# Optimization experiments

Hardware: AMD Instinct MI355X
Metric: run time of the kernel (lower is better)

Reference implementation:

```python
import jax, jax.numpy as jnp
import numpy as np

H, DH, M, ITERS = 8, 64, 256, 6   # heads, dim_head, num_landmarks, pinv iters
DIM = H * DH                      # 512
KERNEL = 33                       # residual depthwise conv kernel


def setup_inputs() -> dict:
    key = jax.random.key(0)
    ks = jax.random.split(key, 5)
    b, n = 2, 8192                # n multiple of M -> no divisibility padding
    x = jax.random.normal(ks[0], (b, n, DIM), jnp.float32)
    ln_gamma = jnp.ones((DIM,), jnp.float32)
    ln_beta = jnp.zeros((DIM,), jnp.float32)
    w_qkv = jax.random.normal(ks[1], (DIM, 3 * DIM), jnp.float32) * 0.02
    w_out = jax.random.normal(ks[2], (DIM, DIM), jnp.float32) * 0.02
    b_out = jnp.zeros((DIM,), jnp.float32)
    res_kernel = jax.random.normal(ks[3], (H, 1, KERNEL, 1), jnp.float32) * 0.02
    return {"x": x, "ln_gamma": ln_gamma, "ln_beta": ln_beta, "w_qkv": w_qkv,
            "w_out": w_out, "b_out": b_out, "res_kernel": res_kernel}


def _pinv(a, iters):
    # lucidrains moore_penrose_iter_pinv (Newton-Schulz iteration)
    abs_a = jnp.abs(a)
    scale = abs_a.sum(-1).max() * abs_a.sum(-2).max()
    z = jnp.swapaxes(a, -1, -2) / scale
    I = jnp.eye(a.shape[-1], dtype=a.dtype)
    for _ in range(iters):
        az = a @ z
        z = 0.25 * z @ (13.0 * I - az @ (15.0 * I - az @ (7.0 * I - az)))
    return z


def reference(x, ln_gamma, ln_beta, w_qkv, w_out, b_out, res_kernel):
    b, n, d = x.shape
    # pre-LayerNorm (eps 1e-5)
    mu = jnp.mean(x, -1, keepdims=True)
    var = jnp.var(x, -1, keepdims=True)
    xn = (x - mu) * jax.lax.rsqrt(var + 1e-5) * ln_gamma + ln_beta
    # qkv projection (bias-free)
    q, k, v = jnp.split(xn @ w_qkv, 3, axis=-1)
    to_heads = lambda t: t.reshape(b, n, H, DH).transpose(0, 2, 1, 3)  # b h n d
    q, k, v = to_heads(q), to_heads(k), to_heads(v)
    q = q * (DH ** -0.5)
    # landmarks: mean over groups of l consecutive tokens ('(m l) d -> m d')
    l = n // M
    q_l = q.reshape(b, H, M, l, DH).mean(3)  # b h M d
    k_l = k.reshape(b, H, M, l, DH).mean(3)
    sim1 = jnp.einsum('bhnd,bhmd->bhnm', q, k_l)      # queries vs k-landmarks
    sim2 = jnp.einsum('bhid,bhjd->bhij', q_l, k_l)    # landmarks vs landmarks
    sim3 = jnp.einsum('bhmd,bhnd->bhmn', q_l, k)      # q-landmarks vs keys
    a1 = jax.nn.softmax(sim1, axis=-1)
    a2 = jax.nn.softmax(sim2, axis=-1)
    a3 = jax.nn.softmax(sim3, axis=-1)
    a2_inv = _pinv(a2, ITERS)
    out = (a1 @ a2_inv) @ (a3 @ v)  # b h n d
    # residual depthwise conv over the sequence axis (Conv2d kernel (33,1), groups=H)
    pad = KERNEL // 2
    out = out + jax.lax.conv_general_dilated(
        v, res_kernel, (1, 1), [(pad, pad), (0, 0)],
        dimension_numbers=('NCHW', 'OIHW', 'NCHW'), feature_group_count=H)
    out = out.transpose(0, 2, 1, 3).reshape(b, n, d)
    out = out @ w_out + b_out  # to_out Linear (dropout inactive at eval)
    return x + out             # TransLayer residual
```

## Files before the change

kernel.cpp:

```cpp
#include <hip/hip_runtime.h>
#include <math.h>

#define H_ 8
#define DH_ 64
#define DIM_ 512
#define M_ 256
#define N_ 8192
#define BH_ 16
#define LG_ 32
#define KC_ 33
#define CH_ 16
#define NTI_ 8

typedef __attribute__((ext_vector_type(8))) short bf16x8;
typedef __attribute__((ext_vector_type(4))) short s16x4;
typedef __attribute__((ext_vector_type(4))) float f32x4;

__device__ __forceinline__ short f2bf(float f) {
  unsigned u = __float_as_uint(f);
  unsigned r = (u + 0x7FFF + ((u >> 16) & 1)) >> 16;
  return (short)r;
}
__device__ __forceinline__ float bf2f(short s) {
  return __uint_as_float(((unsigned)(unsigned short)s) << 16);
}

__device__ __forceinline__ void mfma_nt_core(const short* __restrict__ A,
                                             const short* __restrict__ Bt, int K,
                                             int m0, int n0, size_t lda, size_t ldb,
                                             f32x4 acc[4][4], short* As, short* Bs) {
  const int tid = threadIdx.x;
  const int wave = tid >> 6, lane = tid & 63;
  const int wr = (wave >> 1) * 64, wc = (wave & 1) * 64;
  const int mi = lane & 15, quad = lane >> 4;
  for (int k0 = 0; k0 < K; k0 += 32) {
#pragma unroll
    for (int t = 0; t < 2; ++t) {
      const int cbase = (t * 4 + wave) * 64;
      const int chunk = cbase + lane;
      const int row = chunk >> 2, cc = (chunk & 3) * 8;
      __builtin_amdgcn_global_load_lds(
          (const __attribute__((address_space(1))) void*)(A + (size_t)(m0 + row) * lda + k0 + cc),
          (__attribute__((address_space(3))) void*)(As + (size_t)cbase * 8), 16, 0, 0);
      __builtin_amdgcn_global_load_lds(
          (const __attribute__((address_space(1))) void*)(Bt + (size_t)(n0 + row) * ldb + k0 + cc),
          (__attribute__((address_space(3))) void*)(Bs + (size_t)cbase * 8), 16, 0, 0);
    }
    __syncthreads();
    bf16x8 af[4], bf[4];
#pragma unroll
    for (int i = 0; i < 4; ++i)
      af[i] = *(const bf16x8*)&As[(wr + i * 16 + mi) * 32 + quad * 8];
#pragma unroll
    for (int j = 0; j < 4; ++j)
      bf[j] = *(const bf16x8*)&Bs[(wc + j * 16 + mi) * 32 + quad * 8];
#pragma unroll
    for (int i = 0; i < 4; ++i)
#pragma unroll
      for (int j = 0; j < 4; ++j)
        acc[i][j] = __builtin_amdgcn_mfma_f32_16x16x32_bf16(af[i], bf[j], acc[i][j], 0, 0, 0);
    __syncthreads();
  }
}

__global__ __launch_bounds__(256) void qkv_mfma(const short* __restrict__ xnb,
                                                const short* __restrict__ wt,
                                                short* __restrict__ qb, short* __restrict__ kb,
                                                short* __restrict__ vb) {
  __shared__ short As[128 * 32], Bs[128 * 32];
  f32x4 acc[4][4] = {};
  const int m0 = blockIdx.x * 128, n0 = blockIdx.y * 128;
  mfma_nt_core(xnb, wt, DIM_, m0, n0, DIM_, DIM_, acc, As, Bs);
  const int wave = threadIdx.x >> 6, lane = threadIdx.x & 63;
  const int wr = (wave >> 1) * 64, wc = (wave & 1) * 64;
  const int mi = lane & 15, quad = lane >> 4;
  const int which = n0 >> 9;
  short* dst = which == 0 ? qb : which == 1 ? kb : vb;
  const float sc = which == 0 ? 0.125f : 1.0f;
#pragma unroll
  for (int j = 0; j < 4; ++j) {
    const int col = n0 + wc + j * 16 + mi;
    const int h = (col >> 6) & 7, d = col & 63;
#pragma unroll
    for (int i = 0; i < 4; ++i) {
#pragma unroll
      for (int r = 0; r < 4; ++r) {
        const int row = m0 + wr + i * 16 + quad * 4 + r;
        const int b = row >> 13, t = row & (N_ - 1);
        dst[((size_t)(b * H_ + h) * N_ + t) * DH_ + d] = f2bf(acc[i][j][r] * sc);
      }
    }
  }
}

__global__ __launch_bounds__(256) void final_mfma(const short* __restrict__ omb,
                                                  const short* __restrict__ wt,
                                                  const float* __restrict__ x,
                                                  const float* __restrict__ bout,
                                                  float* __restrict__ y) {
  __shared__ short As[128 * 32], Bs[128 * 32];
  f32x4 acc[4][4] = {};
  const int m0 = blockIdx.x * 128, n0 = blockIdx.y * 128;
  mfma_nt_core(omb, wt, DIM_, m0, n0, DIM_, DIM_, acc, As, Bs);
  const int wave = threadIdx.x >> 6, lane = threadIdx.x & 63;
  const int wr = (wave >> 1) * 64, wc = (wave & 1) * 64;
  const int mi = lane & 15, quad = lane >> 4;
#pragma unroll
  for (int j = 0; j < 4; ++j) {
    const int col = n0 + wc + j * 16 + mi;
    const float bo = bout[col];
#pragma unroll
    for (int i = 0; i < 4; ++i) {
#pragma unroll
      for (int r = 0; r < 4; ++r) {
        const int row = m0 + wr + i * 16 + quad * 4 + r;
        y[(size_t)row * DIM_ + col] = acc[i][j][r] + x[(size_t)row * DIM_ + col] + bo;
      }
    }
  }
}

__global__ __launch_bounds__(256) void convt_kernel(const float* __restrict__ in,
                                                    short* __restrict__ out, int K, int N) {
  __shared__ float tile[32][33];
  const int n0 = blockIdx.x * 32, k0 = blockIdx.y * 32;
  const int tx = threadIdx.x & 31, ty = threadIdx.x >> 5;
  for (int r = ty; r < 32; r += 8) tile[r][tx] = in[(size_t)(k0 + r) * N + n0 + tx];
  __syncthreads();
  for (int r = ty; r < 32; r += 8) out[(size_t)(n0 + r) * K + k0 + tx] = f2bf(tile[tx][r]);
}

__global__ __launch_bounds__(256) void vt_kernel(const short* __restrict__ vb,
                                                 short* __restrict__ vtb) {
  __shared__ short tile[32][33];
  const int t0 = blockIdx.x * 32, d0 = blockIdx.y * 32, bh = blockIdx.z;
  const int tx = threadIdx.x & 31, ty = threadIdx.x >> 5;
  for (int r = ty; r < 32; r += 8)
    tile[r][tx] = vb[((size_t)bh * N_ + t0 + r) * DH_ + d0 + tx];
  __syncthreads();
  for (int r = ty; r < 32; r += 8)
    vtb[((size_t)bh * DH_ + d0 + r) * N_ + t0 + tx] = tile[tx][r];
}

__global__ __launch_bounds__(128) void ln_kernel(const float* __restrict__ x,
                                                 const float* __restrict__ gamma,
                                                 const float* __restrict__ beta,
                                                 short* __restrict__ xnb) {
  const int row = blockIdx.x, tid = threadIdx.x;
  const float4 v = ((const float4*)(x + (size_t)row * DIM_))[tid];
  float s = v.x + v.y + v.z + v.w;
  float ss = v.x * v.x + v.y * v.y + v.z * v.z + v.w * v.w;
  __shared__ float r1[128], r2[128];
  r1[tid] = s;
  r2[tid] = ss;
  __syncthreads();
  for (int off = 64; off > 0; off >>= 1) {
    if (tid < off) {
      r1[tid] += r1[tid + off];
      r2[tid] += r2[tid + off];
    }
    __syncthreads();
  }
  const float mu = r1[0] * (1.0f / DIM_);
  const float var = r2[0] * (1.0f / DIM_) - mu * mu;
  const float rs = rsqrtf(var + 1e-5f);
  const float4 g = ((const float4*)gamma)[tid];
  const float4 bb = ((const float4*)beta)[tid];
  s16x4 o = {f2bf((v.x - mu) * rs * g.x + bb.x), f2bf((v.y - mu) * rs * g.y + bb.y),
             f2bf((v.z - mu) * rs * g.z + bb.z), f2bf((v.w - mu) * rs * g.w + bb.w)};
  ((s16x4*)(xnb + (size_t)row * DIM_))[tid] = o;
}

__global__ __launch_bounds__(256) void landmark_kernel(const short* __restrict__ qb,
                                                       const short* __restrict__ kb,
                                                       float* __restrict__ ql,
                                                       float* __restrict__ kl,
                                                       short* __restrict__ qlb,
                                                       short* __restrict__ klb) {
  const int idx = blockIdx.x * 256 + threadIdx.x;
  const int d = idx & (DH_ - 1);
  const int m = (idx >> 6) & (M_ - 1);
  const int bh = idx >> 14;
  const size_t base = ((size_t)bh * N_ + m * LG_) * DH_ + d;
  float sq = 0.f, sk = 0.f;
#pragma unroll 8
  for (int t = 0; t < LG_; ++t) {
    sq += bf2f(qb[base + (size_t)t * DH_]);
    sk += bf2f(kb[base + (size_t)t * DH_]);
  }
  sq *= (1.0f / LG_);
  sk *= (1.0f / LG_);
  ql[idx] = sq;
  kl[idx] = sk;
  qlb[idx] = f2bf(sq);
  klb[idx] = f2bf(sk);
}

__global__ __launch_bounds__(256) void sim2_softmax(const float* __restrict__ ql,
                                                    const float* __restrict__ kl,
                                                    float* __restrict__ a2,
                                                    short* __restrict__ a2b) {
  const int i = blockIdx.x, bh = blockIdx.y, j = threadIdx.x;
  __shared__ float qrow[DH_];
  if (j < DH_) qrow[j] = ql[((size_t)bh * M_ + i) * DH_ + j];
  __syncthreads();
  const float* kr = kl + ((size_t)bh * M_ + j) * DH_;
  float s = 0.f;
#pragma unroll 16
  for (int d = 0; d < DH_; ++d) s += qrow[d] * kr[d];
  __shared__ float red[256];
  red[j] = s;
  __syncthreads();
  for (int off = 128; off > 0; off >>= 1) {
    if (j < off) red[j] = fmaxf(red[j], red[j + off]);
    __syncthreads();
  }
  const float mx = red[0];
  __syncthreads();
  const float e = expf(s - mx);
  red[j] = e;
  __syncthreads();
  for (int off = 128; off > 0; off >>= 1) {
    if (j < off) red[j] += red[j + off];
    __syncthreads();
  }
  const float out = e / red[0];
  a2[((size_t)bh * M_ + i) * M_ + j] = out;
  a2b[((size_t)bh * M_ + i) * M_ + j] = f2bf(out);
}

__global__ __launch_bounds__(256) void colmax_kernel(const float* __restrict__ a2,
                                                     unsigned int* __restrict__ scalebits) {
  const int bh = blockIdx.x, j = threadIdx.x;
  const float* mat = a2 + (size_t)bh * M_ * M_;
  float s = 0.f;
  for (int i = 0; i < M_; ++i) s += fabsf(mat[i * M_ + j]);
  __shared__ float red[256];
  red[j] = s;
  __syncthreads();
  for (int off = 128; off > 0; off >>= 1) {
    if (j < off) red[j] = fmaxf(red[j], red[j + off]);
    __syncthreads();
  }
  if (j == 0) atomicMax(scalebits, __float_as_uint(red[0]));
}

__global__ __launch_bounds__(256) void transpose_scale(const float* __restrict__ a2,
                                                       short* __restrict__ z0b,
                                                       const unsigned int* __restrict__ scalebits) {
  const float inv = 1.0f / __uint_as_float(*scalebits);
  const int idx = blockIdx.x * 256 + threadIdx.x;
  const int j = idx & (M_ - 1), i = (idx >> 8) & (M_ - 1), bh = idx >> 16;
  z0b[idx] = f2bf(a2[((size_t)bh * M_ + j) * M_ + i] * inv);
}

__device__ __forceinline__ void ns_core(const short* __restrict__ A, const short* __restrict__ B,
                                        int m0, int n0, short* Bs, f32x4 acc[4]) {
  const int tid = threadIdx.x, wave = tid >> 6, lane = tid & 63;
  const int mi = lane & 15, quad = lane >> 4;
  const int bkk = tid & 31, g = tid >> 5;
  bf16x8 bv[8];
#pragma unroll
  for (int kc = 0; kc < 8; ++kc)
    bv[kc] = *(const bf16x8*)(B + (size_t)(kc * 32 + bkk) * M_ + n0 + g * 8);
  const short* arow = A + (size_t)(m0 + wave * 16 + mi) * M_;
  bf16x8 af[8];
#pragma unroll
  for (int k0 = 0; k0 < 8; ++k0)
    af[k0] = *(const bf16x8*)(arow + k0 * 32 + quad * 8);
#pragma unroll
  for (int kc = 0; kc < 8; ++kc)
#pragma unroll
    for (int e = 0; e < 8; ++e)
      Bs[(g * 8 + e) * 260 + kc * 32 + bkk] = bv[kc][e];
  __syncthreads();
#pragma unroll
  for (int k0 = 0; k0 < 8; ++k0) {
#pragma unroll
    for (int j = 0; j < 4; ++j) {
      union { bf16x8 v; s16x4 h[2]; } bfr;
      const short* bp = &Bs[(j * 16 + mi) * 260 + k0 * 32 + quad * 8];
      bfr.h[0] = *(const s16x4*)bp;
      bfr.h[1] = *(const s16x4*)(bp + 4);
      acc[j] = __builtin_amdgcn_mfma_f32_16x16x32_bf16(af[k0], bfr.v, acc[j], 0, 0, 0);
    }
  }
}

__device__ __forceinline__ int ns_remap() {
  const int lin = blockIdx.y * 16 + blockIdx.x;
  return (lin & 7) * (gridDim.y << 1) + (lin >> 3);
}

__global__ __launch_bounds__(256) void ns_gemm0(const short* __restrict__ A,
                                                const short* __restrict__ B,
                                                short* __restrict__ C) {
  __shared__ short Bs[64 * 260];
  const int id = ns_remap();
  const int bx = id & 15, by = id >> 4;
  const int m0 = (bx >> 2) * 64, n0 = (bx & 3) * 64;
  const size_t mo = (size_t)by * (M_ * M_);
  f32x4 acc[4] = {};
  ns_core(A + mo, B + mo, m0, n0, Bs, acc);
  const int wave = threadIdx.x >> 6, lane = threadIdx.x & 63;
  const int mi = lane & 15, quad = lane >> 4;
#pragma unroll
  for (int j = 0; j < 4; ++j)
#pragma unroll
    for (int r = 0; r < 4; ++r) {
      const int row = m0 + wave * 16 + quad * 4 + r, col = n0 + j * 16 + mi;
      C[mo + (size_t)row * M_ + col] = f2bf(acc[j][r]);
    }
}

__global__ __launch_bounds__(256) void ns_stageA(const short* __restrict__ z,
                                                 const short* __restrict__ y,
                                                 short* __restrict__ p1,
                                                 short* __restrict__ y2,
                                                 short* __restrict__ w) {
  __shared__ short Bs[64 * 260];
  const int id = ns_remap();
  const int bx = id & 15, by = id >> 4;
  const int m0 = (bx >> 2) * 64, n0 = (bx & 3) * 64;
  const int sel = by & 1;
  const size_t mo = (size_t)(by >> 1) * (M_ * M_);
  f32x4 acc[4] = {};
  ns_core((sel ? y : z) + mo, y + mo, m0, n0, Bs, acc);
  const int wave = threadIdx.x >> 6, lane = threadIdx.x & 63;
  const int mi = lane & 15, quad = lane >> 4;
#pragma unroll
  for (int j = 0; j < 4; ++j)
#pragma unroll
    for (int r = 0; r < 4; ++r) {
      const int row = m0 + wave * 16 + quad * 4 + r, col = n0 + j * 16 + mi;
      const size_t idx = mo + (size_t)row * M_ + col;
      if (sel) {
        y2[idx] = f2bf(acc[j][r]);
        w[idx] = f2bf(1.75f * bf2f(y[idx]) - 0.25f * acc[j][r]);
      } else {
        p1[idx] = f2bf(acc[j][r]);
      }
    }
}

__global__ __launch_bounds__(256) void ns_stageB(const short* __restrict__ p1,
                                                 const short* __restrict__ y2,
                                                 const short* __restrict__ w,
                                                 const short* __restrict__ z,
                                                 const short* __restrict__ y,
                                                 short* __restrict__ zo,
                                                 short* __restrict__ yo,
                                                 float* __restrict__ zf, int zonly) {
  __shared__ short Bs[64 * 260];
  const int id = ns_remap();
  const int bx = id & 15, by = id >> 4;
  const int m0 = (bx >> 2) * 64, n0 = (bx & 3) * 64;
  const int sel = zonly ? 0 : (by & 1);
  const size_t mo = (size_t)(zonly ? by : (by >> 1)) * (M_ * M_);
  f32x4 acc[4] = {};
  ns_core((sel ? y2 : p1) + mo, w + mo, m0, n0, Bs, acc);
  const int wave = threadIdx.x >> 6, lane = threadIdx.x & 63;
  const int mi = lane & 15, quad = lane >> 4;
#pragma unroll
  for (int j = 0; j < 4; ++j)
#pragma unroll
    for (int r = 0; r < 4; ++r) {
      const int row = m0 + wave * 16 + quad * 4 + r, col = n0 + j * 16 + mi;
      const size_t idx = mo + (size_t)row * M_ + col;
      if (sel) {
        yo[idx] = f2bf(3.25f * bf2f(y[idx]) - 3.75f * bf2f(y2[idx]) + acc[j][r]);
      } else {
        const float v = 3.25f * bf2f(z[idx]) - 3.75f * bf2f(p1[idx]) + acc[j][r];
        zo[idx] = f2bf(v);
        if (zf) zf[idx] = v;
      }
    }
}

__device__ __forceinline__ void mm_step(float (*As)[68], float (*Bs)[68],
                                        int tr, int tc, float acc[4][4]) {
#pragma unroll
  for (int kk = 0; kk < 16; ++kk) {
    const float4 a4 = *(const float4*)&As[kk][tr * 4];
    const float4 b4 = *(const float4*)&Bs[kk][tc * 4];
    const float a[4] = {a4.x, a4.y, a4.z, a4.w};
    const float b[4] = {b4.x, b4.y, b4.z, b4.w};
#pragma unroll
    for (int i = 0; i < 4; ++i)
#pragma unroll
      for (int j = 0; j < 4; ++j) acc[i][j] = fmaf(a[i], b[j], acc[i][j]);
  }
}

__device__ __forceinline__ void load_a_tile(const float* A, int lda, int m0, int k0,
                                            int tid, float (*As)[68]) {
  const int r = tid >> 2, kq = tid & 3;
  const float4 a4 = *(const float4*)(A + (size_t)(m0 + r) * lda + k0 + kq * 4);
  As[kq * 4 + 0][r] = a4.x;
  As[kq * 4 + 1][r] = a4.y;
  As[kq * 4 + 2][r] = a4.z;
  As[kq * 4 + 3][r] = a4.w;
}

__device__ __forceinline__ void load_b_nn(const float* B, int ldb, int k0, int n0,
                                          int tid, float (*Bs)[68]) {
  const int kr = tid >> 4, c4 = tid & 15;
  const float4 b4 = *(const float4*)(B + (size_t)(k0 + kr) * ldb + n0 + c4 * 4);
  *(float4*)&Bs[kr][c4 * 4] = b4;
}

__global__ __launch_bounds__(256) void gemm_nn64(const float* __restrict__ A, int lda,
                                                 long long strideA,
                                                 const float* __restrict__ B, long long strideB,
                                                 float* __restrict__ C, long long strideC,
                                                 int kchunk) {
  const int bz = blockIdx.z;
  A += (size_t)bz * strideA;
  B += (size_t)bz * strideB;
  C += (size_t)bz * strideC;
  const int m0 = blockIdx.x * 64;
  const int tid = threadIdx.x, tr = tid >> 4, tc = tid & 15;
  __shared__ float As[16][68], Bs[16][68];
  float acc[4][4] = {};
  for (int k0 = 0; k0 < kchunk; k0 += 16) {
    load_a_tile(A, lda, m0, k0, tid, As);
    load_b_nn(B, DH_, k0, 0, tid, Bs);
    __syncthreads();
    mm_step(As, Bs, tr, tc, acc);
    __syncthreads();
  }
#pragma unroll
  for (int i = 0; i < 4; ++i) {
    const int row = m0 + tr * 4 + i;
    *(float4*)(C + (size_t)row * DH_ + tc * 4) =
        make_float4(acc[i][0], acc[i][1], acc[i][2], acc[i][3]);
  }
}

__device__ __forceinline__ void stage_ks(const short* __restrict__ kb, int bh, int n0,
                                         int wave, int lane, short* ks) {
#pragma unroll
  for (int i = 0; i < 2; ++i) {
    const int cb = i * 256 + wave * 64;
    const int c = cb + lane;
    const int row = c >> 3, cc = c & 7;
    __builtin_amdgcn_global_load_lds(
        (const __attribute__((address_space(1))) void*)(
            kb + ((size_t)bh * N_ + n0 + row) * DH_ + ((cc ^ (row & 7)) * 8)),
        (__attribute__((address_space(3))) void*)(ks + (size_t)cb * 8), 16, 0, 0);
  }
}

__global__ __launch_bounds__(256) void a3_flash(const short* __restrict__ qlb,
                                                const short* __restrict__ kb,
                                                const short* __restrict__ vtb,
                                                float* __restrict__ Opart,
                                                float* __restrict__ mpart,
                                                float* __restrict__ lpart) {
  const int chunk = blockIdx.x, rt = blockIdx.y, bh = blockIdx.z;
  __shared__ short ks[64 * 64];
  __shared__ short ps[64 * 64];
  const int tid = threadIdx.x, wave = tid >> 6, lane = tid & 63;
  const int mi = lane & 15, quad = lane >> 4;
  const short* qrow = qlb + ((size_t)bh * M_ + rt * 64 + wave * 16 + mi) * DH_;
  const bf16x8 aq0 = *(const bf16x8*)(qrow + quad * 8);
  const bf16x8 aq1 = *(const bf16x8*)(qrow + 32 + quad * 8);
  float m[4] = {-INFINITY, -INFINITY, -INFINITY, -INFINITY};
  float l[4] = {0.f, 0.f, 0.f, 0.f};
  f32x4 o[4] = {};
  stage_ks(kb, bh, chunk * (N_ / CH_), wave, lane, ks);
  __syncthreads();
  for (int t = 0; t < NTI_; ++t) {
    const int n0 = chunk * (N_ / CH_) + t * 64;
    f32x4 s[4];
#pragma unroll
    for (int j = 0; j < 4; ++j) {
      const int row = j * 16 + mi;
      const bf16x8 b0 = *(const bf16x8*)&ks[row * 64 + ((quad ^ (row & 7)) * 8)];
      const bf16x8 b1 = *(const bf16x8*)&ks[row * 64 + (((quad + 4) ^ (row & 7)) * 8)];
      f32x4 z = {0.f, 0.f, 0.f, 0.f};
      z = __builtin_amdgcn_mfma_f32_16x16x32_bf16(aq0, b0, z, 0, 0, 0);
      s[j] = __builtin_amdgcn_mfma_f32_16x16x32_bf16(aq1, b1, z, 0, 0, 0);
    }
    __syncthreads();
    if (t + 1 < NTI_) stage_ks(kb, bh, n0 + 64, wave, lane, ks);
    float alpha[4];
#pragma unroll
    for (int r = 0; r < 4; ++r) {
      float v = fmaxf(fmaxf(s[0][r], s[1][r]), fmaxf(s[2][r], s[3][r]));
      v = fmaxf(v, __shfl_xor(v, 1, 64));
      v = fmaxf(v, __shfl_xor(v, 2, 64));
      v = fmaxf(v, __shfl_xor(v, 4, 64));
      v = fmaxf(v, __shfl_xor(v, 8, 64));
      const float mnew = fmaxf(m[r], v);
      alpha[r] = __expf(m[r] - mnew);
      m[r] = mnew;
    }
    float rs[4] = {0.f, 0.f, 0.f, 0.f};
#pragma unroll
    for (int j = 0; j < 4; ++j)
#pragma unroll
      for (int r = 0; r < 4; ++r) {
        const float p = __expf(s[j][r] - m[r]);
        rs[r] += p;
        const int prow = wave * 16 + quad * 4 + r;
        const int pcol = j * 16 + mi;
        ps[prow * 64 + (((pcol >> 3) ^ (prow & 7)) * 8) + (pcol & 7)] = f2bf(p);
      }
#pragma unroll
    for (int r = 0; r < 4; ++r) {
      float v = rs[r];
      v += __shfl_xor(v, 1, 64);
      v += __shfl_xor(v, 2, 64);
      v += __shfl_xor(v, 4, 64);
      v += __shfl_xor(v, 8, 64);
      l[r] = l[r] * alpha[r] + v;
#pragma unroll
      for (int j = 0; j < 4; ++j) o[j][r] *= alpha[r];
    }
    const int prow = wave * 16 + mi;
    const bf16x8 ap0 = *(const bf16x8*)&ps[prow * 64 + ((quad ^ (mi & 7)) * 8)];
    const bf16x8 ap1 = *(const bf16x8*)&ps[prow * 64 + (((quad + 4) ^ (mi & 7)) * 8)];
#pragma unroll
    for (int j = 0; j < 4; ++j) {
      const short* vp = vtb + ((size_t)bh * DH_ + j * 16 + mi) * N_ + n0;
      const bf16x8 b0 = *(const bf16x8*)(vp + quad * 8);
      const bf16x8 b1 = *(const bf16x8*)(vp + 32 + quad * 8);
      o[j] = __builtin_amdgcn_mfma_f32_16x16x32_bf16(ap0, b0, o[j], 0, 0, 0);
      o[j] = __builtin_amdgcn_mfma_f32_16x16x32_bf16(ap1, b1, o[j], 0, 0, 0);
    }
    __syncthreads();
  }
  const int p2 = bh * 4 + rt;
  float* Ob = Opart + ((size_t)chunk * 64 + p2) * 4096;
#pragma unroll
  for (int j = 0; j < 4; ++j)
#pragma unroll
    for (int r = 0; r < 4; ++r)
      Ob[(wave * 16 + quad * 4 + r) * 64 + j * 16 + mi] = o[j][r];
  if (mi == 0) {
#pragma unroll
    for (int r = 0; r < 4; ++r) {
      mpart[((size_t)chunk * 64 + p2) * 64 + wave * 16 + quad * 4 + r] = m[r];
      lpart[((size_t)chunk * 64 + p2) * 64 + wave * 16 + quad * 4 + r] = l[r];
    }
  }
}

__global__ __launch_bounds__(256) void a3_combine(const float* __restrict__ Opart,
                                                  const float* __restrict__ mpart,
                                                  const float* __restrict__ lpart,
                                                  float* __restrict__ a3v) {
  const int p2 = blockIdx.x, ds = blockIdx.y;
  const int bh = p2 >> 2, rt = p2 & 3;
  __shared__ float wgt[CH_][64];
  const int tid = threadIdx.x;
  if (tid < 64) {
    float mg = -INFINITY;
#pragma unroll
    for (int c = 0; c < CH_; ++c) mg = fmaxf(mg, mpart[((size_t)c * 64 + p2) * 64 + tid]);
    float e[CH_], lg = 0.f;
#pragma unroll
    for (int c = 0; c < CH_; ++c) {
      e[c] = __expf(mpart[((size_t)c * 64 + p2) * 64 + tid] - mg);
      lg += lpart[((size_t)c * 64 + p2) * 64 + tid] * e[c];
    }
    const float inv = 1.f / lg;
#pragma unroll
    for (int c = 0; c < CH_; ++c) wgt[c][tid] = e[c] * inv;
  }
  __syncthreads();
  for (int i = ds * 1024 + tid; i < ds * 1024 + 1024; i += 256) {
    const int row = i >> 6, d = i & 63;
    float s = 0.f;
#pragma unroll
    for (int c = 0; c < CH_; ++c) s += Opart[((size_t)c * 64 + p2) * 4096 + i] * wgt[c][row];
    a3v[((size_t)bh * M_ + rt * 64 + row) * DH_ + d] = s;
  }
}

__global__ __launch_bounds__(256) void w2t_kernel(const float* __restrict__ w2,
                                                  short* __restrict__ w2tb) {
  const int bh = blockIdx.x, tid = threadIdx.x;
  for (int i = tid; i < M_ * DH_; i += 256) {
    const int r = i >> 6, d = i & 63;
    w2tb[((size_t)bh * DH_ + d) * M_ + r] = f2bf(w2[(size_t)bh * M_ * DH_ + i]);
  }
}

__global__ __launch_bounds__(256, 5) void a1_conv(const short* __restrict__ qb,
                                                  const short* __restrict__ klb,
                                                  const short* __restrict__ w2tb,
                                                  const short* __restrict__ vtb,
                                                  const float* __restrict__ rk,
                                                  short* __restrict__ omb) {
  __shared__ __align__(16) char smem[20096];
  short* kls = (short*)smem;
  short* ps = (short*)smem;
  short* vwin = (short*)smem;
  short* band = (short*)(smem + 17920);
  const int bh = blockIdx.y, t0 = blockIdx.x * 64;
  const int b = bh >> 3, h = bh & 7;
  const int tid = threadIdx.x, wave = tid >> 6, lane = tid & 63;
  const int mi = lane & 15, quad = lane >> 4;

  const short* qrow = qb + ((size_t)bh * N_ + t0 + wave * 16 + mi) * DH_;
  const bf16x8 aq0 = *(const bf16x8*)(qrow + quad * 8);
  const bf16x8 aq1 = *(const bf16x8*)(qrow + 32 + quad * 8);

#pragma unroll
  for (int i = 0; i < 4; ++i) {
    const int idx = tid + i * 256;
    const int r = idx >> 6, c = idx & 63, u = c - r;
    band[r * 68 + c] = (u >= 0 && u < KC_) ? f2bf(rk[h * KC_ + u]) : (short)0;
  }

  f32x4 s[16] = {};
#pragma unroll
  for (int half = 0; half < 2; ++half) {
    if (half) __syncthreads();
#pragma unroll
    for (int i = 0; i < 4; ++i) {
      const int cb = i * 256 + wave * 64;
      const int c = cb + lane;
      const int row = c >> 3, cc = c & 7;
      __builtin_amdgcn_global_load_lds(
          (const __attribute__((address_space(1))) void*)(
              klb + ((size_t)bh * M_ + half * 128 + row) * DH_ + (cc ^ (row & 7)) * 8),
          (__attribute__((address_space(3))) void*)(kls + (size_t)cb * 8), 16, 0, 0);
    }
    __syncthreads();
#pragma unroll
    for (int f = 0; f < 8; ++f) {
      const int row = f * 16 + mi;
      const bf16x8 blo = *(const bf16x8*)&kls[row * 64 + ((quad ^ (row & 7)) * 8)];
      const bf16x8 bhi = *(const bf16x8*)&kls[row * 64 + (((quad + 4) ^ (row & 7)) * 8)];
      f32x4 z = __builtin_amdgcn_mfma_f32_16x16x32_bf16(aq0, blo, s[half * 8 + f], 0, 0, 0);
      s[half * 8 + f] = __builtin_amdgcn_mfma_f32_16x16x32_bf16(aq1, bhi, z, 0, 0, 0);
    }
  }
  float inv[4];
#pragma unroll
  for (int r = 0; r < 4; ++r) {
    float v = s[0][r];
#pragma unroll
    for (int f = 1; f < 16; ++f) v = fmaxf(v, s[f][r]);
    v = fmaxf(v, __shfl_xor(v, 1, 64));
    v = fmaxf(v, __shfl_xor(v, 2, 64));
    v = fmaxf(v, __shfl_xor(v, 4, 64));
    v = fmaxf(v, __shfl_xor(v, 8, 64));
    float sum = 0.f;
#pragma unroll
    for (int f = 0; f < 16; ++f) {
      const float p = __expf(s[f][r] - v);
      s[f][r] = p;
      sum += p;
    }
    sum += __shfl_xor(sum, 1, 64);
    sum += __shfl_xor(sum, 2, 64);
    sum += __shfl_xor(sum, 4, 64);
    sum += __shfl_xor(sum, 8, 64);
    inv[r] = 1.f / sum;
  }
  __syncthreads();

  f32x4 o[4] = {};
#pragma unroll
  for (int half = 0; half < 2; ++half) {
#pragma unroll
    for (int f = 0; f < 8; ++f)
#pragma unroll
      for (int r = 0; r < 4; ++r)
        ps[(wave * 16 + quad * 4 + r) * 140 + f * 16 + mi] = f2bf(s[half * 8 + f][r] * inv[r]);
#pragma unroll
    for (int k0 = 0; k0 < 4; ++k0) {
      union { bf16x8 v; s16x4 hh[2]; } ap;
      const short* pp = &ps[(wave * 16 + mi) * 140 + k0 * 32 + quad * 8];
      ap.hh[0] = *(const s16x4*)pp;
      ap.hh[1] = *(const s16x4*)(pp + 4);
#pragma unroll
      for (int j = 0; j < 4; ++j) {
        const bf16x8 bw = *(const bf16x8*)(w2tb + ((size_t)bh * DH_ + j * 16 + mi) * M_ +
                                           (half * 4 + k0) * 32 + quad * 8);
        o[j] = __builtin_amdgcn_mfma_f32_16x16x32_bf16(ap.v, bw, o[j], 0, 0, 0);
      }
    }
  }
  __syncthreads();

  {
    const int d = tid & 63, cg0 = tid >> 6;
    const short* vrow = vtb + ((size_t)bh * DH_ + d) * N_;
    for (int ch = cg0; ch < 14; ch += 4) {
      const int tbase = t0 - 16 + ch * 8;
      bf16x8 vv;
      if (tbase >= 0 && tbase + 8 <= N_) {
        vv = *(const bf16x8*)(vrow + tbase);
      } else {
#pragma unroll
        for (int e = 0; e < 8; ++e) {
          const int tt = tbase + e;
          vv[e] = (tt >= 0 && tt < N_) ? vrow[tt] : (short)0;
        }
      }
      *(bf16x8*)&vwin[d * 116 + ch * 8] = vv;
    }
  }
  __syncthreads();

#pragma unroll
  for (int ks = 0; ks < 2; ++ks) {
    union { bf16x8 v; s16x4 hh[2]; } ab;
    const short* bp = &band[mi * 68 + ks * 32 + quad * 8];
    ab.hh[0] = *(const s16x4*)bp;
    ab.hh[1] = *(const s16x4*)(bp + 4);
#pragma unroll
    for (int j = 0; j < 4; ++j) {
      union { bf16x8 v; s16x4 hh[2]; } bv;
      const short* vp = &vwin[(j * 16 + mi) * 116 + wave * 16 + ks * 32 + quad * 8];
      bv.hh[0] = *(const s16x4*)vp;
      bv.hh[1] = *(const s16x4*)(vp + 4);
      o[j] = __builtin_amdgcn_mfma_f32_16x16x32_bf16(ab.v, bv.v, o[j], 0, 0, 0);
    }
  }
#pragma unroll
  for (int j = 0; j < 4; ++j) {
    const int d = j * 16 + mi;
#pragma unroll
    for (int r = 0; r < 4; ++r) {
      const int t = t0 + wave * 16 + quad * 4 + r;
      omb[((size_t)(b * N_ + t)) * DIM_ + h * DH_ + d] = f2bf(o[j][r]);
    }
  }
}

extern "C" void kernel_launch(void* const* d_in, const int* in_sizes, int n_in,
                              void* d_out, int out_size, void* d_ws, size_t ws_size,
                              hipStream_t stream) {
  (void)in_sizes; (void)n_in; (void)out_size;
  const float* x = (const float*)d_in[0];
  const float* gamma = (const float*)d_in[1];
  const float* beta = (const float*)d_in[2];
  const float* wqkv = (const float*)d_in[3];
  const float* wout = (const float*)d_in[4];
  const float* bout = (const float*)d_in[5];
  const float* rk = (const float*)d_in[6];
  float* y = (float*)d_out;
  float* ws = (float*)d_ws;

  size_t o = 0;
  short* xnb = (short*)(ws + o);   o += (size_t)2 * N_ * DIM_ / 2;
  short* wqkvt = (short*)(ws + o); o += (size_t)3 * DIM_ * DIM_ / 2;
  short* woutt = (short*)(ws + o); o += (size_t)DIM_ * DIM_ / 2;
  short* qb = (short*)(ws + o);    o += (size_t)BH_ * N_ * DH_ / 2;
  short* kb = (short*)(ws + o);    o += (size_t)BH_ * N_ * DH_ / 2;
  short* vb = (short*)(ws + o);    o += (size_t)BH_ * N_ * DH_ / 2;
  short* vtb = (short*)(ws + o);   o += (size_t)BH_ * N_ * DH_ / 2;
  float* ql = ws + o;  o += (size_t)BH_ * M_ * DH_;
  float* kl = ws + o;  o += (size_t)BH_ * M_ * DH_;
  short* qlb = (short*)(ws + o); o += (size_t)BH_ * M_ * DH_ / 2;
  short* klb = (short*)(ws + o); o += (size_t)BH_ * M_ * DH_ / 2;
  float* a2 = ws + o;  o += (size_t)BH_ * M_ * M_;
  float* z0f = ws + o; o += (size_t)BH_ * M_ * M_;
  short* a2b = (short*)(ws + o); o += (size_t)BH_ * M_ * M_ / 2;
  short* zb0 = (short*)(ws + o); o += (size_t)BH_ * M_ * M_ / 2;
  short* zb1 = (short*)(ws + o); o += (size_t)BH_ * M_ * M_ / 2;
  short* yb0 = (short*)(ws + o); o += (size_t)BH_ * M_ * M_ / 2;
  short* yb1 = (short*)(ws + o); o += (size_t)BH_ * M_ * M_ / 2;
  short* p1b = (short*)(ws + o); o += (size_t)BH_ * M_ * M_ / 2;
  short* y2b = (short*)(ws + o); o += (size_t)BH_ * M_ * M_ / 2;
  short* wb  = (short*)(ws + o); o += (size_t)BH_ * M_ * M_ / 2;
  float* Opart = ws + o; o += (size_t)CH_ * 64 * 4096;
  float* mpart = ws + o; o += (size_t)CH_ * 64 * 64;
  float* lpart = ws + o; o += (size_t)CH_ * 64 * 64;
  float* a3v = ws + o; o += (size_t)BH_ * M_ * DH_;
  float* w2 = ws + o;  o += (size_t)BH_ * M_ * DH_;
  short* w2tb = (short*)(ws + o); o += (size_t)BH_ * M_ * DH_ / 2;
  short* omb = (short*)(ws + o);  o += (size_t)2 * N_ * DIM_ / 2;
  unsigned int* scalebits = (unsigned int*)(ws + o); o += 16;
  if (ws_size < o * sizeof(float)) return;

  (void)hipMemsetAsync(scalebits, 0, 64, stream);
  ln_kernel<<<2 * N_, 128, 0, stream>>>(x, gamma, beta, xnb);
  convt_kernel<<<dim3(3 * DIM_ / 32, DIM_ / 32), 256, 0, stream>>>(wqkv, wqkvt, DIM_, 3 * DIM_);
  convt_kernel<<<dim3(DIM_ / 32, DIM_ / 32), 256, 0, stream>>>(wout, woutt, DIM_, DIM_);
  qkv_mfma<<<dim3(2 * N_ / 128, 3 * DIM_ / 128), 256, 0, stream>>>(xnb, wqkvt, qb, kb, vb);
  vt_kernel<<<dim3(N_ / 32, 2, BH_), 256, 0, stream>>>(vb, vtb);

  landmark_kernel<<<BH_ * M_ * DH_ / 256, 256, 0, stream>>>(qb, kb, ql, kl, qlb, klb);
  sim2_softmax<<<dim3(M_, BH_), 256, 0, stream>>>(ql, kl, a2, a2b);
  colmax_kernel<<<BH_, 256, 0, stream>>>(a2, scalebits);
  transpose_scale<<<BH_ * M_ * M_ / 256, 256, 0, stream>>>(a2, zb0, scalebits);

  a3_flash<<<dim3(CH_, 4, BH_), 256, 0, stream>>>(qlb, kb, vtb, Opart, mpart, lpart);
  a3_combine<<<dim3(64, 4), 256, 0, stream>>>(Opart, mpart, lpart, a3v);

  ns_gemm0<<<dim3(16, BH_), 256, 0, stream>>>(a2b, zb0, yb0);
  short* zc = zb0; short* zn = zb1; short* yc = yb0; short* yn = yb1;
  for (int it = 0; it < 6; ++it) {
    const int last = (it == 5);
    ns_stageA<<<dim3(16, 2 * BH_), 256, 0, stream>>>(zc, yc, p1b, y2b, wb);
    ns_stageB<<<dim3(16, last ? BH_ : 2 * BH_), 256, 0, stream>>>(
        p1b, y2b, wb, zc, yc, zn, yn, last ? z0f : nullptr, last);
    short* t;
    t = zc; zc = zn; zn = t;
    t = yc; yc = yn; yn = t;
  }

  gemm_nn64<<<dim3(M_ / 64, 1, BH_), 256, 0, stream>>>(
      z0f, M_, (long long)M_ * M_, a3v, (long long)M_ * DH_, w2, (long long)M_ * DH_, M_);
  w2t_kernel<<<BH_, 256, 0, stream>>>(w2, w2tb);

  a1_conv<<<dim3(N_ / 64, BH_), 256, 0, stream>>>(qb, klb, w2tb, vtb, rk, omb);

  final_mfma<<<dim3(2 * N_ / 128, DIM_ / 128), 256, 0, stream>>>(omb, woutt, x, bout, y);
}
```

Measured before the change: 463.9 us.

## Double-buffer K/V tiles in a3_flash and restructure a1_conv loads and normalization

a3_flash now stages both K and V tiles into double-buffered LDS with async global-to-LDS loads. The next tile is prefetched while the current one is computed, and one barrier per iteration is dropped. The per-iteration row-sum shuffle reduction is deferred to a single reduction after the loop. a1_conv now loads all landmark keys in one pass, prefetches the V window into registers at kernel start, and applies the softmax normalization to the output accumulators instead of to P. This needs more LDS and a lower launch-bounds occupancy hint (5 to 4 blocks) in exchange for fewer barriers and better latency hiding.

Result: faster. 445.1 us (-4.1%).

```diff
diff --git a/kernel.cpp b/kernel.cpp
--- a/kernel.cpp
+++ b/kernel.cpp
@@ -451,6 +451,20 @@
   }
 }
 
+__device__ __forceinline__ void stage_vs(const short* __restrict__ vtb, int bh, int n0,
+                                         int wave, int lane, short* vs) {
+#pragma unroll
+  for (int i = 0; i < 2; ++i) {
+    const int cb = i * 256 + wave * 64;
+    const int c = cb + lane;
+    const int row = c >> 3, cc = c & 7;
+    __builtin_amdgcn_global_load_lds(
+        (const __attribute__((address_space(1))) void*)(
+            vtb + ((size_t)bh * DH_ + row) * N_ + n0 + ((cc ^ (row & 7)) * 8)),
+        (__attribute__((address_space(3))) void*)(vs + (size_t)cb * 8), 16, 0, 0);
+  }
+}
+
 __global__ __launch_bounds__(256) void a3_flash(const short* __restrict__ qlb,
                                                 const short* __restrict__ kb,
                                                 const short* __restrict__ vtb,
@@ -458,7 +472,8 @@
                                                 float* __restrict__ mpart,
                                                 float* __restrict__ lpart) {
   const int chunk = blockIdx.x, rt = blockIdx.y, bh = blockIdx.z;
-  __shared__ short ks[64 * 64];
+  __shared__ short ks[2][64 * 64];
+  __shared__ short vs[2][64 * 64];
   __shared__ short ps[64 * 64];
   const int tid = threadIdx.x, wave = tid >> 6, lane = tid & 63;
   const int mi = lane & 15, quad = lane >> 4;
@@ -468,22 +483,26 @@
   float m[4] = {-INFINITY, -INFINITY, -INFINITY, -INFINITY};
   float l[4] = {0.f, 0.f, 0.f, 0.f};
   f32x4 o[4] = {};
-  stage_ks(kb, bh, chunk * (N_ / CH_), wave, lane, ks);
+  const int nbase = chunk * (N_ / CH_);
+  stage_ks(kb, bh, nbase, wave, lane, ks[0]);
+  stage_vs(vtb, bh, nbase, wave, lane, vs[0]);
   __syncthreads();
   for (int t = 0; t < NTI_; ++t) {
-    const int n0 = chunk * (N_ / CH_) + t * 64;
+    const int cur = t & 1;
+    if (t + 1 < NTI_) {
+      stage_ks(kb, bh, nbase + (t + 1) * 64, wave, lane, ks[cur ^ 1]);
+      stage_vs(vtb, bh, nbase + (t + 1) * 64, wave, lane, vs[cur ^ 1]);
+    }
     f32x4 s[4];
 #pragma unroll
     for (int j = 0; j < 4; ++j) {
       const int row = j * 16 + mi;
-      const bf16x8 b0 = *(const bf16x8*)&ks[row * 64 + ((quad ^ (row & 7)) * 8)];
-      const bf16x8 b1 = *(const bf16x8*)&ks[row * 64 + (((quad + 4) ^ (row & 7)) * 8)];
+      const bf16x8 b0 = *(const bf16x8*)&ks[cur][row * 64 + ((quad ^ (row & 7)) * 8)];
+      const bf16x8 b1 = *(const bf16x8*)&ks[cur][row * 64 + (((quad + 4) ^ (row & 7)) * 8)];
       f32x4 z = {0.f, 0.f, 0.f, 0.f};
       z = __builtin_amdgcn_mfma_f32_16x16x32_bf16(aq0, b0, z, 0, 0, 0);
       s[j] = __builtin_amdgcn_mfma_f32_16x16x32_bf16(aq1, b1, z, 0, 0, 0);
     }
-    __syncthreads();
-    if (t + 1 < NTI_) stage_ks(kb, bh, n0 + 64, wave, lane, ks);
     float alpha[4];
 #pragma unroll
     for (int r = 0; r < 4; ++r) {
@@ -509,12 +528,7 @@
       }
 #pragma unroll
     for (int r = 0; r < 4; ++r) {
-      float v = rs[r];
-      v += __shfl_xor(v, 1, 64);
-      v += __shfl_xor(v, 2, 64);
-      v += __shfl_xor(v, 4, 64);
-      v += __shfl_xor(v, 8, 64);
-      l[r] = l[r] * alpha[r] + v;
+      l[r] = l[r] * alpha[r] + rs[r];
 #pragma unroll
       for (int j = 0; j < 4; ++j) o[j][r] *= alpha[r];
     }
@@ -523,13 +537,22 @@
     const bf16x8 ap1 = *(const bf16x8*)&ps[prow * 64 + (((quad + 4) ^ (mi & 7)) * 8)];
 #pragma unroll
     for (int j = 0; j < 4; ++j) {
-      const short* vp = vtb + ((size_t)bh * DH_ + j * 16 + mi) * N_ + n0;
-      const bf16x8 b0 = *(const bf16x8*)(vp + quad * 8);
-      const bf16x8 b1 = *(const bf16x8*)(vp + 32 + quad * 8);
+      const int vrow = j * 16 + mi;
+      const bf16x8 b0 = *(const bf16x8*)&vs[cur][vrow * 64 + ((quad ^ (vrow & 7)) * 8)];
+      const bf16x8 b1 = *(const bf16x8*)&vs[cur][vrow * 64 + (((quad + 4) ^ (vrow & 7)) * 8)];
       o[j] = __builtin_amdgcn_mfma_f32_16x16x32_bf16(ap0, b0, o[j], 0, 0, 0);
       o[j] = __builtin_amdgcn_mfma_f32_16x16x32_bf16(ap1, b1, o[j], 0, 0, 0);
     }
     __syncthreads();
+  }
+#pragma unroll
+  for (int r = 0; r < 4; ++r) {
+    float v = l[r];
+    v += __shfl_xor(v, 1, 64);
+    v += __shfl_xor(v, 2, 64);
+    v += __shfl_xor(v, 4, 64);
+    v += __shfl_xor(v, 8, 64);
+    l[r] = v;
   }
   const int p2 = bh * 4 + rt;
   float* Ob = Opart + ((size_t)chunk * 64 + p2) * 4096;
@@ -588,17 +611,17 @@
   }
 }
 
-__global__ __launch_bounds__(256, 5) void a1_conv(const short* __restrict__ qb,
+__global__ __launch_bounds__(256, 4) void a1_conv(const short* __restrict__ qb,
                                                   const short* __restrict__ klb,
                                                   const short* __restrict__ w2tb,
                                                   const short* __restrict__ vtb,
                                                   const float* __restrict__ rk,
                                                   short* __restrict__ omb) {
-  __shared__ __align__(16) char smem[20096];
+  __shared__ __align__(16) char smem[34944];
   short* kls = (short*)smem;
   short* ps = (short*)smem;
-  short* vwin = (short*)smem;
-  short* band = (short*)(smem + 17920);
+  short* vwin = (short*)(smem + 17920);
+  short* band = (short*)(smem + 32768);
   const int bh = blockIdx.y, t0 = blockIdx.x * 64;
   const int b = bh >> 3, h = bh & 7;
   const int tid = threadIdx.x, wave = tid >> 6, lane = tid & 63;
@@ -608,6 +631,29 @@
   const bf16x8 aq0 = *(const bf16x8*)(qrow + quad * 8);
   const bf16x8 aq1 = *(const bf16x8*)(qrow + 32 + quad * 8);
 
+  const int vd = tid & 63, cg0 = tid >> 6;
+  bf16x8 vreg[4];
+  {
+    const short* vrow = vtb + ((size_t)bh * DH_ + vd) * N_;
+#pragma unroll
+    for (int slot = 0; slot < 4; ++slot) {
+      const int ch = cg0 + slot * 4;
+      bf16x8 vv = {};
+      if (ch < 14) {
+        const int tbase = t0 - 16 + ch * 8;
+        if (tbase >= 0 && tbase + 8 <= N_) {
+          vv = *(const bf16x8*)(vrow + tbase);
+        } else {
+#pragma unroll
+          for (int e = 0; e < 8; ++e) {
+            const int tt = tbase + e;
+            vv[e] = (tt >= 0 && tt < N_) ? vrow[tt] : (short)0;
+          }
+        }
+      }
+      vreg[slot] = vv;
+    }
+  }
 #pragma unroll
   for (int i = 0; i < 4; ++i) {
     const int idx = tid + i * 256;
@@ -615,31 +661,28 @@
     band[r * 68 + c] = (u >= 0 && u < KC_) ? f2bf(rk[h * KC_ + u]) : (short)0;
   }
 
+#pragma unroll
+  for (int i = 0; i < 8; ++i) {
+    const int cb = i * 256 + wave * 64;
+    const int c = cb + lane;
+    const int row = c >> 3, cc = c & 7;
+    __builtin_amdgcn_global_load_lds(
+        (const __attribute__((address_space(1))) void*)(
+            klb + ((size_t)bh * M_ + row) * DH_ + (cc ^ (row & 7)) * 8),
+        (__attribute__((address_space(3))) void*)(kls + (size_t)cb * 8), 16, 0, 0);
+  }
+  __syncthreads();
+
   f32x4 s[16] = {};
 #pragma unroll
-  for (int half = 0; half < 2; ++half) {
-    if (half) __syncthreads();
-#pragma unroll
-    for (int i = 0; i < 4; ++i) {
-      const int cb = i * 256 + wave * 64;
-      const int c = cb + lane;
-      const int row = c >> 3, cc = c & 7;
-      __builtin_amdgcn_global_load_lds(
-          (const __attribute__((address_space(1))) void*)(
-              klb + ((size_t)bh * M_ + half * 128 + row) * DH_ + (cc ^ (row & 7)) * 8),
-          (__attribute__((address_space(3))) void*)(kls + (size_t)cb * 8), 16, 0, 0);
-    }
-    __syncthreads();
-#pragma unroll
-    for (int f = 0; f < 8; ++f) {
-      const int row = f * 16 + mi;
-      const bf16x8 blo = *(const bf16x8*)&kls[row * 64 + ((quad ^ (row & 7)) * 8)];
-      const bf16x8 bhi = *(const bf16x8*)&kls[row * 64 + (((quad + 4) ^ (row & 7)) * 8)];
-      f32x4 z = __builtin_amdgcn_mfma_f32_16x16x32_bf16(aq0, blo, s[half * 8 + f], 0, 0, 0);
-      s[half * 8 + f] = __builtin_amdgcn_mfma_f32_16x16x32_bf16(aq1, bhi, z, 0, 0, 0);
-    }
-  }
-  float inv[4];
+  for (int f = 0; f < 16; ++f) {
+    const int row = f * 16 + mi;
+    const bf16x8 blo = *(const bf16x8*)&kls[row * 64 + ((quad ^ (row & 7)) * 8)];
+    const bf16x8 bhi = *(const bf16x8*)&kls[row * 64 + (((quad + 4) ^ (row & 7)) * 8)];
+    f32x4 z = __builtin_amdgcn_mfma_f32_16x16x32_bf16(aq0, blo, s[f], 0, 0, 0);
+    s[f] = __builtin_amdgcn_mfma_f32_16x16x32_bf16(aq1, bhi, z, 0, 0, 0);
+  }
+  float lsum[4];
 #pragma unroll
   for (int r = 0; r < 4; ++r) {
     float v = s[0][r];
@@ -656,13 +699,15 @@
       s[f][r] = p;
       sum += p;
     }
-    sum += __shfl_xor(sum, 1, 64);
-    sum += __shfl_xor(sum, 2, 64);
-    sum += __shfl_xor(sum, 4, 64);
-    sum += __shfl_xor(sum, 8, 64);
-    inv[r] = 1.f / sum;
-  }
-  __syncthreads();
+    lsum[r] = sum;
+  }
+  __syncthreads();
+
+#pragma unroll
+  for (int slot = 0; slot < 4; ++slot) {
+    const int ch = cg0 + slot * 4;
+    if (ch < 14) *(bf16x8*)&vwin[vd * 116 + ch * 8] = vreg[slot];
+  }
 
   f32x4 o[4] = {};
 #pragma unroll
@@ -671,7 +716,7 @@
     for (int f = 0; f < 8; ++f)
 #pragma unroll
       for (int r = 0; r < 4; ++r)
-        ps[(wave * 16 + quad * 4 + r) * 140 + f * 16 + mi] = f2bf(s[half * 8 + f][r] * inv[r]);
+        ps[(wave * 16 + quad * 4 + r) * 140 + f * 16 + mi] = f2bf(s[half * 8 + f][r]);
 #pragma unroll
     for (int k0 = 0; k0 < 4; ++k0) {
       union { bf16x8 v; s16x4 hh[2]; } ap;
@@ -686,25 +731,16 @@
       }
     }
   }
-  __syncthreads();
-
-  {
-    const int d = tid & 63, cg0 = tid >> 6;
-    const short* vrow = vtb + ((size_t)bh * DH_ + d) * N_;
-    for (int ch = cg0; ch < 14; ch += 4) {
-      const int tbase = t0 - 16 + ch * 8;
-      bf16x8 vv;
-      if (tbase >= 0 && tbase + 8 <= N_) {
-        vv = *(const bf16x8*)(vrow + tbase);
-      } else {
-#pragma unroll
-        for (int e = 0; e < 8; ++e) {
-          const int tt = tbase + e;
-          vv[e] = (tt >= 0 && tt < N_) ? vrow[tt] : (short)0;
-        }
-      }
-      *(bf16x8*)&vwin[d * 116 + ch * 8] = vv;
-    }
+#pragma unroll
+  for (int r = 0; r < 4; ++r) {
+    float v = lsum[r];
+    v += __shfl_xor(v, 1, 64);
+    v += __shfl_xor(v, 2, 64);
+    v += __shfl_xor(v, 4, 64);
+    v += __shfl_xor(v, 8, 64);
+    const float inv = 1.f / v;
+#pragma unroll
+    for (int j = 0; j < 4; ++j) o[j][r] *= inv;
   }
   __syncthreads();
 
```
